# Optimization experiments

Measured on AMD Instinct MI355X. Metric: run time of the kernel, lower is better.

The kernel has to match this reference:

```python
import jax, jax.numpy as jnp
import numpy as np

B, N, H = 4, 256, 512
P = 128  # game_physics_params


def _init(key, shape, scale=0.02):
    return jax.random.normal(key, shape, dtype=jnp.float32) * scale


def setup_inputs() -> dict:
    key = jax.random.key(0)
    ks = jax.random.split(key, 16)
    return {
        "object_features": jax.random.normal(ks[0], (B, N, H), dtype=jnp.float32),
        # physics_predictor: H -> 512 -> P
        "pp_w1": _init(ks[1], (H, 512)), "pp_b1": jnp.zeros((512,), jnp.float32),
        "pp_w2": _init(ks[2], (512, P)), "pp_b2": jnp.zeros((P,), jnp.float32),
        # collision_detector: 2H -> 256 -> 128 -> 1
        "cd_w1": _init(ks[3], (2 * H, 256)), "cd_b1": jnp.zeros((256,), jnp.float32),
        "cd_w2": _init(ks[4], (256, 128)), "cd_b2": jnp.zeros((128,), jnp.float32),
        "cd_w3": _init(ks[5], (128, 1)), "cd_b3": jnp.zeros((1,), jnp.float32),
        # velocity / force heads: H -> 3
        "vel_w": _init(ks[6], (H, 3)), "vel_b": jnp.zeros((3,), jnp.float32),
        "frc_w": _init(ks[7], (H, 3)), "frc_b": jnp.zeros((3,), jnp.float32),
    }


def reference(object_features, pp_w1, pp_b1, pp_w2, pp_b2,
              cd_w1, cd_b1, cd_w2, cd_b2, cd_w3, cd_b3,
              vel_w, vel_b, frc_w, frc_b):
    x = object_features  # [B, N, H]
    # physics predictor MLP
    p = jax.nn.relu(x @ pp_w1 + pp_b1) @ pp_w2 + pp_b2  # [B, N, P]
    mass = jax.nn.sigmoid(p[..., 0:1]) * 100.0
    friction = jax.nn.sigmoid(p[..., 1:2])
    elasticity = jax.nn.sigmoid(p[..., 2:3])
    density = jax.nn.sigmoid(p[..., 3:4]) * 10.0
    velocities = x @ vel_w + vel_b  # [B, N, 3]
    forces = x @ frc_w + frc_b      # [B, N, 3]

    # vectorized pairwise collision detection over upper-triangle pairs
    iu, ju = np.triu_indices(N, k=1)  # static index arrays, length Np = N(N-1)/2
    pairs = jnp.concatenate([x[:, iu], x[:, ju]], axis=-1)  # [B, Np, 2H]
    h = jax.nn.relu(pairs @ cd_w1 + cd_b1)
    h = jax.nn.relu(h @ cd_w2 + cd_b2)
    prob = jax.nn.sigmoid(h @ cd_w3 + cd_b3)[..., 0]  # [B, Np]
    collision_matrix = jnp.zeros((x.shape[0], N, N), dtype=x.dtype)
    collision_matrix = collision_matrix.at[:, iu, ju].set(prob).at[:, ju, iu].set(prob)

    return (mass, friction, elasticity, density, velocities, forces, collision_matrix)
```

## Files before the change

### kernel.cpp

```cpp
#include <hip/hip_runtime.h>
#include <hip/hip_bf16.h>

typedef __attribute__((ext_vector_type(8))) short bf16x8;
typedef __attribute__((ext_vector_type(4))) float f32x4;

__device__ __forceinline__ float sigmoidf_(float v) {
    return 1.0f / (1.0f + __expf(-v));
}
__device__ __forceinline__ short f2bf(float f) {
    union { __hip_bfloat16 h; short s; } cv;
    cv.h = __float2bfloat16(f);
    return cv.s;
}
__device__ __forceinline__ float bf2f(short s) {
    union { float f; unsigned u; } cv;
    cv.u = ((unsigned)(unsigned short)s) << 16;
    return cv.f;
}

__global__ __launch_bounds__(256) void convert_kernel(
    const float* __restrict__ x, const float* __restrict__ pp_w1,
    const float* __restrict__ cd_w1, const float* __restrict__ cd_w2,
    const float* __restrict__ pp_w2, const float* __restrict__ vel_w,
    const float* __restrict__ frc_w,
    __hip_bfloat16* __restrict__ xb, __hip_bfloat16* __restrict__ Wt,
    __hip_bfloat16* __restrict__ w2t, float* __restrict__ hw)
{
    __shared__ float ts[64][65];
    const int b = blockIdx.x, t = threadIdx.x;

    if (b < 256) {
        int base = b * 2048 + t * 8;
        float4 a = *(const float4*)(x + base);
        float4 c = *(const float4*)(x + base + 4);
        bf16x8 o;
        o[0] = f2bf(a.x); o[1] = f2bf(a.y); o[2] = f2bf(a.z); o[3] = f2bf(a.w);
        o[4] = f2bf(c.x); o[5] = f2bf(c.y); o[6] = f2bf(c.z); o[7] = f2bf(c.w);
        *(bf16x8*)(xb + base) = o;
        return;
    }
    if (b == 392) {
        for (int e = t; e < 5120; e += 256) {
            int h = e >> 9, k = e & 511;
            float v = (h < 4) ? pp_w2[k * 128 + h]
                    : (h < 7) ? vel_w[k * 3 + (h - 4)]
                              : frc_w[k * 3 + (h - 7)];
            hw[e] = v;
        }
        return;
    }

    const float* src; int ss, k0, n0, region;
    if (b < 320)      { int i = b - 256; src = pp_w1; ss = 512; k0 = (i >> 3) * 64; n0 = (i & 7) * 64; region = 0; }
    else if (b < 384) { int i = b - 320; src = cd_w1; ss = 256; k0 = (i >> 2) * 64; n0 = (i & 3) * 64; region = 1; }
    else              { int i = b - 384; src = cd_w2; ss = 128; k0 = (i >> 1) * 64; n0 = (i & 1) * 64; region = 2; }

    #pragma unroll
    for (int i = 0; i < 4; ++i) {
        int r = (t >> 4) + i * 16, c4 = (t & 15) * 4;
        *(float4*)&ts[r][c4] = *(const float4*)(src + (k0 + r) * ss + n0 + c4);
    }
    __syncthreads();
    #pragma unroll
    for (int i = 0; i < 4; ++i) {
        int nOut = (t >> 4) + i * 16, kc = (t & 15) * 4;
        ushort4 o;
        o.x = (unsigned short)f2bf(ts[kc + 0][nOut]);
        o.y = (unsigned short)f2bf(ts[kc + 1][nOut]);
        o.z = (unsigned short)f2bf(ts[kc + 2][nOut]);
        o.w = (unsigned short)f2bf(ts[kc + 3][nOut]);
        int gn = n0 + nOut, gk = k0 + kc;
        if (region == 0)      *(ushort4*)(Wt + gn * 512 + gk) = o;
        else if (region == 1) {
            int row = (gk < 512) ? (512 + gn) : (768 + gn);
            *(ushort4*)(Wt + row * 512 + (gk & 511)) = o;
        } else                *(ushort4*)(w2t + gn * 256 + gk) = o;
    }
}

__global__ __launch_bounds__(256) void gemm_kernel(
    const __hip_bfloat16* __restrict__ xb, const __hip_bfloat16* __restrict__ Wt,
    const float* __restrict__ pp_b1, const float* __restrict__ cd_b1,
    __hip_bfloat16* __restrict__ hidg, float* __restrict__ Ug,
    float* __restrict__ Vg)
{
    const int t = threadIdx.x;
    const int wave = t >> 6, lane = t & 63;
    const int l = lane & 15, q = lane >> 4;
    const int m0 = blockIdx.y * 32;
    const int n0 = blockIdx.x * 128 + wave * 32;

    const __hip_bfloat16* a0p = xb + (m0 + l) * 512 + q * 8;
    const __hip_bfloat16* a1p = a0p + 16 * 512;
    const __hip_bfloat16* b0p = Wt + (n0 + l) * 512 + q * 8;
    const __hip_bfloat16* b1p = b0p + 16 * 512;

    f32x4 acc00 = {}, acc01 = {}, acc10 = {}, acc11 = {};
    #pragma unroll
    for (int ks = 0; ks < 16; ++ks) {
        bf16x8 a0 = *(const bf16x8*)(a0p + ks * 32);
        bf16x8 a1 = *(const bf16x8*)(a1p + ks * 32);
        bf16x8 b0 = *(const bf16x8*)(b0p + ks * 32);
        bf16x8 b1 = *(const bf16x8*)(b1p + ks * 32);
        acc00 = __builtin_amdgcn_mfma_f32_16x16x32_bf16(a0, b0, acc00, 0, 0, 0);
        acc01 = __builtin_amdgcn_mfma_f32_16x16x32_bf16(a0, b1, acc01, 0, 0, 0);
        acc10 = __builtin_amdgcn_mfma_f32_16x16x32_bf16(a1, b0, acc10, 0, 0, 0);
        acc11 = __builtin_amdgcn_mfma_f32_16x16x32_bf16(a1, b1, acc11, 0, 0, 0);
    }

    const int c0 = n0 + l, c1 = n0 + 16 + l;
    #pragma unroll
    for (int mt = 0; mt < 2; ++mt) {
        const f32x4& A0 = mt ? acc10 : acc00;
        const f32x4& A1 = mt ? acc11 : acc01;
        if (n0 < 512) {
            float b0v = pp_b1[c0], b1v = pp_b1[c1];
            #pragma unroll
            for (int r = 0; r < 4; ++r) {
                int rg = m0 + mt * 16 + q * 4 + r;
                hidg[rg * 512 + c0] = __float2bfloat16(fmaxf(A0[r] + b0v, 0.f));
                hidg[rg * 512 + c1] = __float2bfloat16(fmaxf(A1[r] + b1v, 0.f));
            }
        } else if (n0 < 768) {
            float b0v = cd_b1[c0 - 512], b1v = cd_b1[c1 - 512];
            #pragma unroll
            for (int r = 0; r < 4; ++r) {
                int rg = m0 + mt * 16 + q * 4 + r;
                Ug[rg * 256 + (c0 - 512)] = A0[r] + b0v;
                Ug[rg * 256 + (c1 - 512)] = A1[r] + b1v;
            }
        } else {
            #pragma unroll
            for (int r = 0; r < 4; ++r) {
                int rg = m0 + mt * 16 + q * 4 + r;
                Vg[rg * 256 + (c0 - 768)] = A0[r];
                Vg[rg * 256 + (c1 - 768)] = A1[r];
            }
        }
    }
}

__global__ __launch_bounds__(256) void heads_kernel(
    const float* __restrict__ x, const __hip_bfloat16* __restrict__ hidg,
    const float* __restrict__ hw, const float* __restrict__ pp_b2,
    const float* __restrict__ vel_b, const float* __restrict__ frc_b,
    float* __restrict__ out)
{
    const int t = threadIdx.x, wave = t >> 6, lane = t & 63;
    const int row = blockIdx.x * 4 + wave;

    const float4* xr = (const float4*)(x + row * 512);
    float4 xa = xr[lane * 2], xc = xr[lane * 2 + 1];
    bf16x8 hb = *(const bf16x8*)(hidg + row * 512 + lane * 8);
    float hf[8];
    #pragma unroll
    for (int j = 0; j < 8; ++j) hf[j] = bf2f(hb[j]);

    #pragma unroll
    for (int h = 0; h < 10; ++h) {
        const float4* wr = (const float4*)(hw + h * 512);
        float4 wa = wr[lane * 2], wc = wr[lane * 2 + 1];
        float s;
        if (h < 4) {
            s = hf[0]*wa.x + hf[1]*wa.y + hf[2]*wa.z + hf[3]*wa.w
              + hf[4]*wc.x + hf[5]*wc.y + hf[6]*wc.z + hf[7]*wc.w;
        } else {
            s = xa.x*wa.x + xa.y*wa.y + xa.z*wa.z + xa.w*wa.w
              + xc.x*wc.x + xc.y*wc.y + xc.z*wc.z + xc.w*wc.w;
        }
        s += __shfl_xor(s, 1);  s += __shfl_xor(s, 2);
        s += __shfl_xor(s, 4);  s += __shfl_xor(s, 8);
        s += __shfl_xor(s, 16); s += __shfl_xor(s, 32);
        if (lane == 0) {
            if (h < 4) {
                float sg = sigmoidf_(s + pp_b2[h]);
                out[h * 1024 + row] = (h == 0) ? sg * 100.f : (h == 3) ? sg * 10.f : sg;
            } else if (h < 7) {
                out[4096 + row * 3 + (h - 4)] = s + vel_b[h - 4];
            } else {
                out[7168 + row * 3 + (h - 7)] = s + frc_b[h - 7];
            }
        }
    }
}

__global__ __launch_bounds__(256) void pair_kernel(
    const float* __restrict__ Ug, const float* __restrict__ Vg,
    const __hip_bfloat16* __restrict__ w2t,
    const float* __restrict__ cd_b2, const float* __restrict__ cd_w3,
    const float* __restrict__ cd_b3, float* __restrict__ cm)
{
    const int b = blockIdx.y;
    const int tp = blockIdx.x;
    int ti = (int)((65.0f - sqrtf(4225.0f - 8.0f * (float)tp)) * 0.5f);
    while ((ti + 1) * (65 - (ti + 1)) / 2 <= tp) ++ti;
    while (ti * (65 - ti) / 2 > tp) --ti;
    const int tj = ti + (tp - ti * (65 - ti) / 2);

    __shared__ __align__(16) float Us[8][264];
    __shared__ __align__(16) float Vs[8][264];
    __shared__ float ps[64][4];

    const int t = threadIdx.x;
    const int i0 = ti * 8, j0 = tj * 8;

    {
        const float4* Ug4 = (const float4*)(Ug + (b * 256 + i0) * 256);
        const float4* Vg4 = (const float4*)(Vg + (b * 256 + j0) * 256);
        #pragma unroll
        for (int c = t; c < 512; c += 256) {
            int row = c >> 6, col = (c & 63) << 2;
            *(float4*)&Us[row][col] = Ug4[c];
            *(float4*)&Vs[row][col] = Vg4[c];
        }
    }
    __syncthreads();

    const int wave = t >> 6, lane = t & 63;
    const int l = lane & 15, q = lane >> 4;
    const int pj = l & 7, piB = l >> 3;

    const __hip_bfloat16* wb0 = w2t + ((wave * 2 + 0) * 16 + l) * 256 + q * 8;
    const __hip_bfloat16* wb1 = wb0 + 16 * 256;

    f32x4 acc[4][2] = {};
    #pragma unroll
    for (int ks = 0; ks < 8; ++ks) {
        bf16x8 bfr0 = *(const bf16x8*)(wb0 + ks * 32);
        bf16x8 bfr1 = *(const bf16x8*)(wb1 + ks * 32);
        const int kk = ks * 32 + q * 8;
        #pragma unroll
        for (int mt = 0; mt < 4; ++mt) {
            const int pi = mt * 2 + piB;
            float4 u0 = *(const float4*)&Us[pi][kk];
            float4 u1 = *(const float4*)&Us[pi][kk + 4];
            float4 v0 = *(const float4*)&Vs[pj][kk];
            float4 v1 = *(const float4*)&Vs[pj][kk + 4];
            bf16x8 afr;
            afr[0] = f2bf(fmaxf(u0.x + v0.x, 0.f));
            afr[1] = f2bf(fmaxf(u0.y + v0.y, 0.f));
            afr[2] = f2bf(fmaxf(u0.z + v0.z, 0.f));
            afr[3] = f2bf(fmaxf(u0.w + v0.w, 0.f));
            afr[4] = f2bf(fmaxf(u1.x + v1.x, 0.f));
            afr[5] = f2bf(fmaxf(u1.y + v1.y, 0.f));
            afr[6] = f2bf(fmaxf(u1.z + v1.z, 0.f));
            afr[7] = f2bf(fmaxf(u1.w + v1.w, 0.f));
            acc[mt][0] = __builtin_amdgcn_mfma_f32_16x16x32_bf16(afr, bfr0, acc[mt][0], 0, 0, 0);
            acc[mt][1] = __builtin_amdgcn_mfma_f32_16x16x32_bf16(afr, bfr1, acc[mt][1], 0, 0, 0);
        }
    }

    float b2v0 = cd_b2[(wave * 2 + 0) * 16 + l], b2v1 = cd_b2[(wave * 2 + 1) * 16 + l];
    float w3v0 = cd_w3[(wave * 2 + 0) * 16 + l], w3v1 = cd_w3[(wave * 2 + 1) * 16 + l];
    #pragma unroll
    for (int mt = 0; mt < 4; ++mt) {
        #pragma unroll
        for (int r = 0; r < 4; ++r) {
            float g0 = fmaxf(acc[mt][0][r] + b2v0, 0.f);
            float g1 = fmaxf(acc[mt][1][r] + b2v1, 0.f);
            float s = g0 * w3v0 + g1 * w3v1;
            s += __shfl_xor(s, 1);
            s += __shfl_xor(s, 2);
            s += __shfl_xor(s, 4);
            s += __shfl_xor(s, 8);
            if (l == 0) ps[mt * 16 + q * 4 + r][wave] = s;
        }
    }
    __syncthreads();

    if (t < 64) {
        int p = t;
        float v = ps[p][0] + ps[p][1] + ps[p][2] + ps[p][3] + cd_b3[0];
        float prob = 1.0f / (1.0f + __expf(-v));
        int i = i0 + (p >> 3), j = j0 + (p & 7);
        float* base = cm + b * 65536;
        if (i < j) {
            base[i * 256 + j] = prob;
            base[j * 256 + i] = prob;
        } else if (i == j) {
            base[i * 256 + i] = 0.0f;
        }
    }
}

extern "C" void kernel_launch(void* const* d_in, const int* in_sizes, int n_in,
                              void* d_out, int out_size, void* d_ws, size_t ws_size,
                              hipStream_t stream) {
    const float* x     = (const float*)d_in[0];
    const float* pp_w1 = (const float*)d_in[1];
    const float* pp_b1 = (const float*)d_in[2];
    const float* pp_w2 = (const float*)d_in[3];
    const float* pp_b2 = (const float*)d_in[4];
    const float* cd_w1 = (const float*)d_in[5];
    const float* cd_b1 = (const float*)d_in[6];
    const float* cd_w2 = (const float*)d_in[7];
    const float* cd_b2 = (const float*)d_in[8];
    const float* cd_w3 = (const float*)d_in[9];
    const float* cd_b3 = (const float*)d_in[10];
    const float* vel_w = (const float*)d_in[11];
    const float* vel_b = (const float*)d_in[12];
    const float* frc_w = (const float*)d_in[13];
    const float* frc_b = (const float*)d_in[14];

    float* out = (float*)d_out;
    float* Ug = (float*)d_ws;
    float* Vg = Ug + 262144;
    __hip_bfloat16* xb   = (__hip_bfloat16*)(Vg + 262144);
    __hip_bfloat16* Wt   = xb + 524288;
    __hip_bfloat16* hidg = Wt + 524288;
    __hip_bfloat16* w2t  = hidg + 524288;
    float* hw = (float*)(w2t + 32768);

    convert_kernel<<<dim3(393), dim3(256), 0, stream>>>(
        x, pp_w1, cd_w1, cd_w2, pp_w2, vel_w, frc_w, xb, Wt, w2t, hw);
    gemm_kernel<<<dim3(8, 32), dim3(256), 0, stream>>>(
        xb, Wt, pp_b1, cd_b1, hidg, Ug, Vg);
    heads_kernel<<<dim3(256), dim3(256), 0, stream>>>(
        x, hidg, hw, pp_b2, vel_b, frc_b, out);
    pair_kernel<<<dim3(528, 4), dim3(256), 0, stream>>>(
        Ug, Vg, w2t, cd_b2, cd_w3, cd_b3, out + 10240);
}
```

Baseline: 134.2 us.

## Precompute pair hidden tile in LDS as bf16 and halve GEMM row tile

```diff
diff --git a/kernel.cpp b/kernel.cpp
--- a/kernel.cpp
+++ b/kernel.cpp
@@ -87,55 +87,46 @@
     const int t = threadIdx.x;
     const int wave = t >> 6, lane = t & 63;
     const int l = lane & 15, q = lane >> 4;
-    const int m0 = blockIdx.y * 32;
+    const int m0 = blockIdx.y * 16;
     const int n0 = blockIdx.x * 128 + wave * 32;
 
-    const __hip_bfloat16* a0p = xb + (m0 + l) * 512 + q * 8;
-    const __hip_bfloat16* a1p = a0p + 16 * 512;
+    const __hip_bfloat16* ap  = xb + (m0 + l) * 512 + q * 8;
     const __hip_bfloat16* b0p = Wt + (n0 + l) * 512 + q * 8;
     const __hip_bfloat16* b1p = b0p + 16 * 512;
 
-    f32x4 acc00 = {}, acc01 = {}, acc10 = {}, acc11 = {};
+    f32x4 acc0 = {}, acc1 = {};
     #pragma unroll
     for (int ks = 0; ks < 16; ++ks) {
-        bf16x8 a0 = *(const bf16x8*)(a0p + ks * 32);
-        bf16x8 a1 = *(const bf16x8*)(a1p + ks * 32);
+        bf16x8 a  = *(const bf16x8*)(ap  + ks * 32);
         bf16x8 b0 = *(const bf16x8*)(b0p + ks * 32);
         bf16x8 b1 = *(const bf16x8*)(b1p + ks * 32);
-        acc00 = __builtin_amdgcn_mfma_f32_16x16x32_bf16(a0, b0, acc00, 0, 0, 0);
-        acc01 = __builtin_amdgcn_mfma_f32_16x16x32_bf16(a0, b1, acc01, 0, 0, 0);
-        acc10 = __builtin_amdgcn_mfma_f32_16x16x32_bf16(a1, b0, acc10, 0, 0, 0);
-        acc11 = __builtin_amdgcn_mfma_f32_16x16x32_bf16(a1, b1, acc11, 0, 0, 0);
+        acc0 = __builtin_amdgcn_mfma_f32_16x16x32_bf16(a, b0, acc0, 0, 0, 0);
+        acc1 = __builtin_amdgcn_mfma_f32_16x16x32_bf16(a, b1, acc1, 0, 0, 0);
     }
 
     const int c0 = n0 + l, c1 = n0 + 16 + l;
-    #pragma unroll
-    for (int mt = 0; mt < 2; ++mt) {
-        const f32x4& A0 = mt ? acc10 : acc00;
-        const f32x4& A1 = mt ? acc11 : acc01;
-        if (n0 < 512) {
-            float b0v = pp_b1[c0], b1v = pp_b1[c1];
-            #pragma unroll
-            for (int r = 0; r < 4; ++r) {
-                int rg = m0 + mt * 16 + q * 4 + r;
-                hidg[rg * 512 + c0] = __float2bfloat16(fmaxf(A0[r] + b0v, 0.f));
-                hidg[rg * 512 + c1] = __float2bfloat16(fmaxf(A1[r] + b1v, 0.f));
-            }
-        } else if (n0 < 768) {
-            float b0v = cd_b1[c0 - 512], b1v = cd_b1[c1 - 512];
-            #pragma unroll
-            for (int r = 0; r < 4; ++r) {
-                int rg = m0 + mt * 16 + q * 4 + r;
-                Ug[rg * 256 + (c0 - 512)] = A0[r] + b0v;
-                Ug[rg * 256 + (c1 - 512)] = A1[r] + b1v;
-            }
-        } else {
-            #pragma unroll
-            for (int r = 0; r < 4; ++r) {
-                int rg = m0 + mt * 16 + q * 4 + r;
-                Vg[rg * 256 + (c0 - 768)] = A0[r];
-                Vg[rg * 256 + (c1 - 768)] = A1[r];
-            }
+    if (n0 < 512) {
+        float b0v = pp_b1[c0], b1v = pp_b1[c1];
+        #pragma unroll
+        for (int r = 0; r < 4; ++r) {
+            int rg = m0 + q * 4 + r;
+            hidg[rg * 512 + c0] = __float2bfloat16(fmaxf(acc0[r] + b0v, 0.f));
+            hidg[rg * 512 + c1] = __float2bfloat16(fmaxf(acc1[r] + b1v, 0.f));
+        }
+    } else if (n0 < 768) {
+        float b0v = cd_b1[c0 - 512], b1v = cd_b1[c1 - 512];
+        #pragma unroll
+        for (int r = 0; r < 4; ++r) {
+            int rg = m0 + q * 4 + r;
+            Ug[rg * 256 + (c0 - 512)] = acc0[r] + b0v;
+            Ug[rg * 256 + (c1 - 512)] = acc1[r] + b1v;
+        }
+    } else {
+        #pragma unroll
+        for (int r = 0; r < 4; ++r) {
+            int rg = m0 + q * 4 + r;
+            Vg[rg * 256 + (c0 - 768)] = acc0[r];
+            Vg[rg * 256 + (c1 - 768)] = acc1[r];
         }
     }
 }
@@ -197,28 +188,39 @@
     while (ti * (65 - ti) / 2 > tp) --ti;
     const int tj = ti + (tp - ti * (65 - ti) / 2);
 
-    __shared__ __align__(16) float Us[8][264];
-    __shared__ __align__(16) float Vs[8][264];
+    __shared__ __align__(16) short hs[64][264];
     __shared__ float ps[64][4];
 
     const int t = threadIdx.x;
     const int i0 = ti * 8, j0 = tj * 8;
 
     {
-        const float4* Ug4 = (const float4*)(Ug + (b * 256 + i0) * 256);
-        const float4* Vg4 = (const float4*)(Vg + (b * 256 + j0) * 256);
-        #pragma unroll
-        for (int c = t; c < 512; c += 256) {
-            int row = c >> 6, col = (c & 63) << 2;
-            *(float4*)&Us[row][col] = Ug4[c];
-            *(float4*)&Vs[row][col] = Vg4[c];
+        const int p = t & 63, pi = p >> 3, pj = p & 7;
+        const int kb = (t >> 6) * 64;
+        const float* Up = Ug + (b * 256 + i0 + pi) * 256 + kb;
+        const float* Vp = Vg + (b * 256 + j0 + pj) * 256 + kb;
+        #pragma unroll
+        for (int kk = 0; kk < 64; kk += 8) {
+            float4 u0 = *(const float4*)(Up + kk);
+            float4 u1 = *(const float4*)(Up + kk + 4);
+            float4 v0 = *(const float4*)(Vp + kk);
+            float4 v1 = *(const float4*)(Vp + kk + 4);
+            bf16x8 pack;
+            pack[0] = f2bf(fmaxf(u0.x + v0.x, 0.f));
+            pack[1] = f2bf(fmaxf(u0.y + v0.y, 0.f));
+            pack[2] = f2bf(fmaxf(u0.z + v0.z, 0.f));
+            pack[3] = f2bf(fmaxf(u0.w + v0.w, 0.f));
+            pack[4] = f2bf(fmaxf(u1.x + v1.x, 0.f));
+            pack[5] = f2bf(fmaxf(u1.y + v1.y, 0.f));
+            pack[6] = f2bf(fmaxf(u1.z + v1.z, 0.f));
+            pack[7] = f2bf(fmaxf(u1.w + v1.w, 0.f));
+            *(bf16x8*)&hs[p][kb + kk] = pack;
         }
     }
     __syncthreads();
 
     const int wave = t >> 6, lane = t & 63;
     const int l = lane & 15, q = lane >> 4;
-    const int pj = l & 7, piB = l >> 3;
 
     const __hip_bfloat16* wb0 = w2t + ((wave * 2 + 0) * 16 + l) * 256 + q * 8;
     const __hip_bfloat16* wb1 = wb0 + 16 * 256;
@@ -228,23 +230,9 @@
     for (int ks = 0; ks < 8; ++ks) {
         bf16x8 bfr0 = *(const bf16x8*)(wb0 + ks * 32);
         bf16x8 bfr1 = *(const bf16x8*)(wb1 + ks * 32);
-        const int kk = ks * 32 + q * 8;
         #pragma unroll
         for (int mt = 0; mt < 4; ++mt) {
-            const int pi = mt * 2 + piB;
-            float4 u0 = *(const float4*)&Us[pi][kk];
-            float4 u1 = *(const float4*)&Us[pi][kk + 4];
-            float4 v0 = *(const float4*)&Vs[pj][kk];
-            float4 v1 = *(const float4*)&Vs[pj][kk + 4];
-            bf16x8 afr;
-            afr[0] = f2bf(fmaxf(u0.x + v0.x, 0.f));
-            afr[1] = f2bf(fmaxf(u0.y + v0.y, 0.f));
-            afr[2] = f2bf(fmaxf(u0.z + v0.z, 0.f));
-            afr[3] = f2bf(fmaxf(u0.w + v0.w, 0.f));
-            afr[4] = f2bf(fmaxf(u1.x + v1.x, 0.f));
-            afr[5] = f2bf(fmaxf(u1.y + v1.y, 0.f));
-            afr[6] = f2bf(fmaxf(u1.z + v1.z, 0.f));
-            afr[7] = f2bf(fmaxf(u1.w + v1.w, 0.f));
+            bf16x8 afr = *(const bf16x8*)&hs[mt * 16 + l][ks * 32 + q * 8];
             acc[mt][0] = __builtin_amdgcn_mfma_f32_16x16x32_bf16(afr, bfr0, acc[mt][0], 0, 0, 0);
             acc[mt][1] = __builtin_amdgcn_mfma_f32_16x16x32_bf16(afr, bfr1, acc[mt][1], 0, 0, 0);
         }
@@ -313,7 +301,7 @@
 
     convert_kernel<<<dim3(393), dim3(256), 0, stream>>>(
         x, pp_w1, cd_w1, cd_w2, pp_w2, vel_w, frc_w, xb, Wt, w2t, hw);
-    gemm_kernel<<<dim3(8, 32), dim3(256), 0, stream>>>(
+    gemm_kernel<<<dim3(8, 64), dim3(256), 0, stream>>>(
         xb, Wt, pp_b1, cd_b1, hidg, Ug, Vg);
     heads_kernel<<<dim3(256), dim3(256), 0, stream>>>(
         x, hidg, hw, pp_b2, vel_b, frc_b, out);
```

Result: slower. 155.8 us (+16.1%).

## Enlarge pair tiles to 16x16 and give each wave all hidden columns

Applied to the files above, without the earlier changes.

```diff
diff --git a/kernel.cpp b/kernel.cpp
--- a/kernel.cpp
+++ b/kernel.cpp
@@ -192,50 +192,48 @@
 {
     const int b = blockIdx.y;
     const int tp = blockIdx.x;
-    int ti = (int)((65.0f - sqrtf(4225.0f - 8.0f * (float)tp)) * 0.5f);
-    while ((ti + 1) * (65 - (ti + 1)) / 2 <= tp) ++ti;
-    while (ti * (65 - ti) / 2 > tp) --ti;
-    const int tj = ti + (tp - ti * (65 - ti) / 2);
-
-    __shared__ __align__(16) float Us[8][264];
-    __shared__ __align__(16) float Vs[8][264];
-    __shared__ float ps[64][4];
+    int ti = 0;
+    while ((ti + 1) * (33 - (ti + 1)) / 2 <= tp) ++ti;
+    const int tj = ti + (tp - ti * (33 - ti) / 2);
+
+    __shared__ __align__(16) float Us[16][260];
+    __shared__ __align__(16) float Vs[16][260];
 
     const int t = threadIdx.x;
-    const int i0 = ti * 8, j0 = tj * 8;
+    const int i0 = ti * 16, j0 = tj * 16;
 
     {
-        const float4* Ug4 = (const float4*)(Ug + (b * 256 + i0) * 256);
-        const float4* Vg4 = (const float4*)(Vg + (b * 256 + j0) * 256);
+        const int row = t >> 4, c0 = (t & 15) * 16;
+        const float* Up = Ug + (b * 256 + i0 + row) * 256 + c0;
+        const float* Vp = Vg + (b * 256 + j0 + row) * 256 + c0;
         #pragma unroll
-        for (int c = t; c < 512; c += 256) {
-            int row = c >> 6, col = (c & 63) << 2;
-            *(float4*)&Us[row][col] = Ug4[c];
-            *(float4*)&Vs[row][col] = Vg4[c];
+        for (int i = 0; i < 4; ++i) {
+            *(float4*)&Us[row][c0 + i * 4] = *(const float4*)(Up + i * 4);
+            *(float4*)&Vs[row][c0 + i * 4] = *(const float4*)(Vp + i * 4);
         }
     }
     __syncthreads();
 
     const int wave = t >> 6, lane = t & 63;
     const int l = lane & 15, q = lane >> 4;
-    const int pj = l & 7, piB = l >> 3;
-
-    const __hip_bfloat16* wb0 = w2t + ((wave * 2 + 0) * 16 + l) * 256 + q * 8;
-    const __hip_bfloat16* wb1 = wb0 + 16 * 256;
-
-    f32x4 acc[4][2] = {};
+
+    f32x4 acc[4][8] = {};
+    const __hip_bfloat16* wB = w2t + l * 256 + q * 8;
+
     #pragma unroll
     for (int ks = 0; ks < 8; ++ks) {
-        bf16x8 bfr0 = *(const bf16x8*)(wb0 + ks * 32);
-        bf16x8 bfr1 = *(const bf16x8*)(wb1 + ks * 32);
+        bf16x8 bfr[8];
+        #pragma unroll
+        for (int nt = 0; nt < 8; ++nt)
+            bfr[nt] = *(const bf16x8*)(wB + nt * 16 * 256 + ks * 32);
         const int kk = ks * 32 + q * 8;
         #pragma unroll
         for (int mt = 0; mt < 4; ++mt) {
-            const int pi = mt * 2 + piB;
-            float4 u0 = *(const float4*)&Us[pi][kk];
-            float4 u1 = *(const float4*)&Us[pi][kk + 4];
-            float4 v0 = *(const float4*)&Vs[pj][kk];
-            float4 v1 = *(const float4*)&Vs[pj][kk + 4];
+            const int mtg = wave * 4 + mt;
+            float4 u0 = *(const float4*)&Us[mtg][kk];
+            float4 u1 = *(const float4*)&Us[mtg][kk + 4];
+            float4 v0 = *(const float4*)&Vs[l][kk];
+            float4 v1 = *(const float4*)&Vs[l][kk + 4];
             bf16x8 afr;
             afr[0] = f2bf(fmaxf(u0.x + v0.x, 0.f));
             afr[1] = f2bf(fmaxf(u0.y + v0.y, 0.f));
@@ -245,40 +243,44 @@
             afr[5] = f2bf(fmaxf(u1.y + v1.y, 0.f));
             afr[6] = f2bf(fmaxf(u1.z + v1.z, 0.f));
             afr[7] = f2bf(fmaxf(u1.w + v1.w, 0.f));
-            acc[mt][0] = __builtin_amdgcn_mfma_f32_16x16x32_bf16(afr, bfr0, acc[mt][0], 0, 0, 0);
-            acc[mt][1] = __builtin_amdgcn_mfma_f32_16x16x32_bf16(afr, bfr1, acc[mt][1], 0, 0, 0);
-        }
-    }
-
-    float b2v0 = cd_b2[(wave * 2 + 0) * 16 + l], b2v1 = cd_b2[(wave * 2 + 1) * 16 + l];
-    float w3v0 = cd_w3[(wave * 2 + 0) * 16 + l], w3v1 = cd_w3[(wave * 2 + 1) * 16 + l];
+            #pragma unroll
+            for (int nt = 0; nt < 8; ++nt)
+                acc[mt][nt] = __builtin_amdgcn_mfma_f32_16x16x32_bf16(
+                    afr, bfr[nt], acc[mt][nt], 0, 0, 0);
+        }
+    }
+
+    float b2v[8], w3v[8];
+    #pragma unroll
+    for (int nt = 0; nt < 8; ++nt) {
+        b2v[nt] = cd_b2[nt * 16 + l];
+        w3v[nt] = cd_w3[nt * 16 + l];
+    }
+    const float b3 = cd_b3[0];
+    float* base = cm + b * 65536;
     #pragma unroll
     for (int mt = 0; mt < 4; ++mt) {
+        const int i = i0 + wave * 4 + mt;
         #pragma unroll
         for (int r = 0; r < 4; ++r) {
-            float g0 = fmaxf(acc[mt][0][r] + b2v0, 0.f);
-            float g1 = fmaxf(acc[mt][1][r] + b2v1, 0.f);
-            float s = g0 * w3v0 + g1 * w3v1;
+            float s = 0.f;
+            #pragma unroll
+            for (int nt = 0; nt < 8; ++nt)
+                s += fmaxf(acc[mt][nt][r] + b2v[nt], 0.f) * w3v[nt];
             s += __shfl_xor(s, 1);
             s += __shfl_xor(s, 2);
             s += __shfl_xor(s, 4);
             s += __shfl_xor(s, 8);
-            if (l == 0) ps[mt * 16 + q * 4 + r][wave] = s;
-        }
-    }
-    __syncthreads();
-
-    if (t < 64) {
-        int p = t;
-        float v = ps[p][0] + ps[p][1] + ps[p][2] + ps[p][3] + cd_b3[0];
-        float prob = 1.0f / (1.0f + __expf(-v));
-        int i = i0 + (p >> 3), j = j0 + (p & 7);
-        float* base = cm + b * 65536;
-        if (i < j) {
-            base[i * 256 + j] = prob;
-            base[j * 256 + i] = prob;
-        } else if (i == j) {
-            base[i * 256 + i] = 0.0f;
+            if (l == 0) {
+                const int j = j0 + q * 4 + r;
+                float prob = sigmoidf_(s + b3);
+                if (i < j) {
+                    base[i * 256 + j] = prob;
+                    base[j * 256 + i] = prob;
+                } else if (i == j) {
+                    base[i * 256 + i] = 0.0f;
+                }
+            }
         }
     }
 }
@@ -317,6 +319,6 @@
         xb, Wt, pp_b1, cd_b1, hidg, Ug, Vg);
     heads_kernel<<<dim3(256), dim3(256), 0, stream>>>(
         x, hidg, hw, pp_b2, vel_b, frc_b, out);
-    pair_kernel<<<dim3(528, 4), dim3(256), 0, stream>>>(
+    pair_kernel<<<dim3(136, 4), dim3(256), 0, stream>>>(
         Ug, Vg, w2t, cd_b2, cd_w3, cd_b3, out + 10240);
 }
```

After: 144.3 us. 7.5% more time.
